# Performance work log

Measured on AMD Instinct MI355X. Metric: run time of the kernel, lower is better.

The kernel has to match this reference:

```python
import jax, jax.numpy as jnp
import numpy as np

N_SHOTS, N_SAMPLES, IMG = 10, 192, 256
M = N_SHOTS * N_SAMPLES  # 1920 k-space samples


def _radial_traj():
    # mri-nufft initialize_2D_radial: uniform spoke angles over pi,
    # radii in [-0.5, 0.5) with N_SAMPLES points per spoke.
    r = (np.arange(N_SAMPLES) - N_SAMPLES / 2) / N_SAMPLES
    ang = np.pi * np.arange(N_SHOTS) / N_SHOTS
    kx = np.cos(ang)[:, None] * r[None, :]
    ky = np.sin(ang)[:, None] * r[None, :]
    return np.stack([kx, ky], axis=-1).reshape(-1, 2).astype(np.float32)


def _phase_mats(samples):
    # Separable NDFT phase factors: exp(-2i*pi*k_x*i), exp(-2i*pi*k_y*j)
    grid = jnp.arange(IMG, dtype=jnp.float32) - IMG / 2  # centered pixel coords
    Ax = jnp.exp(-2j * jnp.pi * samples[:, 0:1] * grid[None, :]).astype(jnp.complex64)  # (M, IMG)
    Ay = jnp.exp(-2j * jnp.pi * samples[:, 1:2] * grid[None, :]).astype(jnp.complex64)  # (M, IMG)
    return Ax, Ay


def _pipe_density(samples, n_iter=10):
    # Pipe & Menon density compensation: w <- w / |F F^H w| (density=True in gpunufft).
    Ax, Ay = _phase_mats(samples)
    w = jnp.ones(M, jnp.complex64)
    for _ in range(n_iter):
        t = Ax.conj() * w[:, None]                    # (M, IMG)
        img = jnp.einsum('mi,mj->ij', t, Ay.conj())   # F^H w, (IMG, IMG)
        back = jnp.einsum('mi,ij,mj->m', Ax, img, Ay) # F F^H w, (M,)
        w = w / jnp.maximum(jnp.abs(back), 1e-12).astype(jnp.complex64)
    return jnp.abs(w).astype(jnp.float32)


def setup_inputs() -> dict:
    key = jax.random.key(0)
    k1, k2 = jax.random.split(key)
    B, C = 64, 1
    x_real = jax.random.normal(k1, (B, C, IMG, IMG), dtype=jnp.float32)
    x_imag = jax.random.normal(k2, (B, C, IMG, IMG), dtype=jnp.float32)
    samples = jnp.asarray(_radial_traj())
    density = _pipe_density(samples)
    return {"x_real": x_real, "x_imag": x_imag, "samples": samples, "density": density}


def reference(x_real, x_imag, samples, density):
    x = (x_real + 1j * x_imag).astype(jnp.complex64)  # (B, C, IMG, IMG)
    Ax, Ay = _phase_mats(samples)
    # Forward NUFFT (type-2 NDFT): kspace[b,c,m] = sum_ij Ax[m,i] Ay[m,j] x[b,c,i,j]
    t = jnp.einsum('mi,bcij->bcmj', Ax, x)            # (B, C, M, IMG)
    kspace = jnp.einsum('mj,bcmj->bcm', Ay, t)        # (B, C, M)
    # Density-compensated adjoint NUFFT (type-1 NDFT)
    kw = kspace * density.astype(jnp.complex64)
    u = jnp.einsum('mi,bcm->bcmi', Ax.conj(), kw)     # (B, C, M, IMG)
    adj = jnp.einsum('mj,bcmi->bcij', Ay.conj(), u) / (IMG * IMG)
    return jnp.stack([adj.real, adj.imag], axis=-1)   # (B, C, IMG, IMG, 2)
```

## Files before the change

kernel.cpp:

```cpp
#include <hip/hip_runtime.h>
#include <hip/hip_fp16.h>

constexpr int IMG_ = 256;
constexpr int M_   = 1920;
constexpr int B_   = 64;
constexpr int MI_  = M_ * IMG_;
constexpr int IMG2 = IMG_ * IMG_;

typedef _Float16 half8 __attribute__((ext_vector_type(8)));
typedef float floatx16 __attribute__((ext_vector_type(16)));

__device__ inline void gl_lds16(const void* g, void* l) {
  __builtin_amdgcn_global_load_lds(
      (const __attribute__((address_space(1))) unsigned int*)g,
      (__attribute__((address_space(3))) unsigned int*)l, 16, 0, 0);
}

__global__ __launch_bounds__(256) void phase1_k(
    const float* __restrict__ samples,
    _Float16* __restrict__ axh_r, _Float16* __restrict__ axh_i,
    _Float16* __restrict__ ayh_r, _Float16* __restrict__ ayh_i) {
  int idx = blockIdx.x * 256 + threadIdx.x;
  if (idx >= MI_) return;
  int m = idx >> 8;
  int i = idx & 255;
  float g  = (float)i - 128.0f;
  float kx = samples[2 * m + 0];
  float ky = samples[2 * m + 1];
  float sx, cx, sy, cy;
  sincospif(-2.0f * kx * g, &sx, &cx);
  sincospif(-2.0f * ky * g, &sy, &cy);
  axh_r[idx] = (_Float16)cx; axh_i[idx] = (_Float16)sx;
  ayh_r[idx] = (_Float16)cy; ayh_i[idx] = (_Float16)sy;
}

__global__ __launch_bounds__(256) void phase2_k(
    const float* __restrict__ samples,
    _Float16* __restrict__ axtc_r, _Float16* __restrict__ axtc_i,
    _Float16* __restrict__ aytc_r, _Float16* __restrict__ aytc_i) {
  int m = blockIdx.x * 256 + threadIdx.x;
  if (m >= M_) return;
  int i = blockIdx.y;
  float g  = (float)i - 128.0f;
  float kx = samples[2 * m + 0];
  float ky = samples[2 * m + 1];
  float sx, cx, sy, cy;
  sincospif(-2.0f * kx * g, &sx, &cx);
  sincospif(-2.0f * ky * g, &sy, &cy);
  int o = i * M_ + m;
  axtc_r[o] = (_Float16)cx; axtc_i[o] = (_Float16)(-sx);
  aytc_r[o] = (_Float16)cy; aytc_i[o] = (_Float16)(-sy);
}

__global__ __launch_bounds__(256) void xcvt_k(
    const float* __restrict__ xr, const float* __restrict__ xi,
    _Float16* __restrict__ xh_r, _Float16* __restrict__ xh_i) {
  int idx = (blockIdx.x * 256 + threadIdx.x) * 8;
  float4 a = *(const float4*)&xr[idx];
  float4 c = *(const float4*)&xr[idx + 4];
  half8 h;
  h[0] = (_Float16)a.x; h[1] = (_Float16)a.y; h[2] = (_Float16)a.z; h[3] = (_Float16)a.w;
  h[4] = (_Float16)c.x; h[5] = (_Float16)c.y; h[6] = (_Float16)c.z; h[7] = (_Float16)c.w;
  *(half8*)&xh_r[idx] = h;
  a = *(const float4*)&xi[idx];
  c = *(const float4*)&xi[idx + 4];
  h[0] = (_Float16)a.x; h[1] = (_Float16)a.y; h[2] = (_Float16)a.z; h[3] = (_Float16)a.w;
  h[4] = (_Float16)c.x; h[5] = (_Float16)c.y; h[6] = (_Float16)c.z; h[7] = (_Float16)c.w;
  *(half8*)&xh_i[idx] = h;
}

__global__ __launch_bounds__(256, 2) void fwd_k(
    const _Float16* __restrict__ axh_r, const _Float16* __restrict__ axh_i,
    const _Float16* __restrict__ ayh_r, const _Float16* __restrict__ ayh_i,
    const _Float16* __restrict__ xh_r, const _Float16* __restrict__ xh_i,
    const float* __restrict__ density,
    _Float16* __restrict__ kwh_r, _Float16* __restrict__ kwh_i) {
  __shared__ _Float16 sA[2][2 * 128 * 32];
  __shared__ _Float16 sB[2][2 * 128 * 32];
  __shared__ float kred[2][128][2];

  const int t  = threadIdx.x;
  const int w  = t >> 6, l = t & 63;
  const int lo = l & 31, hi = l >> 5;
  const int mw  = (w & 1) * 64;
  const int iwb = w >> 1;
  const int iw  = iwb * 64;
  const int m0 = blockIdx.x * 128;
  const int b  = blockIdx.y;

  ((float*)kred)[t]       = 0.f;
  ((float*)kred)[t + 256] = 0.f;

  const _Float16* __restrict__ xbr = xh_r + (size_t)b * IMG2;
  const _Float16* __restrict__ xbi = xh_i + (size_t)b * IMG2;

  const floatx16 z16 = {0.f,0.f,0.f,0.f,0.f,0.f,0.f,0.f,0.f,0.f,0.f,0.f,0.f,0.f,0.f,0.f};
  floatx16 accr[2][2], acci[2][2];

  auto stage = [&](int kt, int buf, int ic) {
    const int j0 = kt * 32;
#pragma unroll
    for (int p = 0; p < 2; ++p) {
      int s  = w * 2 + p;
      int q  = s * 64 + l;
      int r  = q >> 2;
      int cl = (q & 3) ^ (r & 3);
      int ga = (m0 + r) * IMG_ + j0 + cl * 8;
      int gb = (ic * 128 + r) * IMG_ + j0 + cl * 8;
      gl_lds16(ayh_r + ga, &sA[buf][s * 512]);
      gl_lds16(ayh_i + ga, &sA[buf][4096 + s * 512]);
      gl_lds16(xbr + gb,  &sB[buf][s * 512]);
      gl_lds16(xbi + gb,  &sB[buf][4096 + s * 512]);
    }
  };

  auto compute = [&](int buf) {
#pragma unroll
    for (int ks = 0; ks < 2; ++ks) {
      half8 ar[2], ai[2], nai[2], br[2], bi[2];
#pragma unroll
      for (int tm = 0; tm < 2; ++tm) {
        int rt  = mw + tm * 32 + lo;
        int off = rt * 32 + ((ks * 2 + hi) ^ (rt & 3)) * 8;
        ar[tm]  = *(const half8*)&sA[buf][off];
        ai[tm]  = *(const half8*)&sA[buf][4096 + off];
        nai[tm] = -ai[tm];
      }
#pragma unroll
      for (int ti = 0; ti < 2; ++ti) {
        int rt  = iw + ti * 32 + lo;
        int off = rt * 32 + ((ks * 2 + hi) ^ (rt & 3)) * 8;
        br[ti]  = *(const half8*)&sB[buf][off];
        bi[ti]  = *(const half8*)&sB[buf][4096 + off];
      }
#pragma unroll
      for (int tm = 0; tm < 2; ++tm)
#pragma unroll
        for (int ti = 0; ti < 2; ++ti) {
          accr[tm][ti] = __builtin_amdgcn_mfma_f32_32x32x16_f16(ar[tm],  br[ti], accr[tm][ti], 0, 0, 0);
          accr[tm][ti] = __builtin_amdgcn_mfma_f32_32x32x16_f16(nai[tm], bi[ti], accr[tm][ti], 0, 0, 0);
          acci[tm][ti] = __builtin_amdgcn_mfma_f32_32x32x16_f16(ar[tm],  bi[ti], acci[tm][ti], 0, 0, 0);
          acci[tm][ti] = __builtin_amdgcn_mfma_f32_32x32x16_f16(ai[tm],  br[ti], acci[tm][ti], 0, 0, 0);
        }
    }
  };

  for (int ic = 0; ic < 2; ++ic) {
#pragma unroll
    for (int tm = 0; tm < 2; ++tm)
#pragma unroll
      for (int ti = 0; ti < 2; ++ti) { accr[tm][ti] = z16; acci[tm][ti] = z16; }

    stage(0, 0, ic);
    for (int kt = 0; kt < 8; kt += 2) {
      __syncthreads();
      stage(kt + 1, 1, ic);
      compute(0);
      __syncthreads();
      if (kt + 2 < 8) stage(kt + 2, 0, ic);
      compute(1);
    }

#pragma unroll
    for (int tm = 0; tm < 2; ++tm) {
#pragma unroll
      for (int reg = 0; reg < 16; ++reg) {
        int row = (reg & 3) + 8 * (reg >> 2) + 4 * hi;
        int m = m0 + mw + tm * 32 + row;
        float wr = 0.f, wi = 0.f;
#pragma unroll
        for (int ti = 0; ti < 2; ++ti) {
          int i = ic * 128 + iw + ti * 32 + lo;
          float xr_ = (float)axh_r[m * IMG_ + i];
          float xi_ = (float)axh_i[m * IMG_ + i];
          float tr = accr[tm][ti][reg], tv = acci[tm][ti][reg];
          wr = fmaf(xr_, tr, fmaf(-xi_, tv, wr));
          wi = fmaf(xr_, tv, fmaf(xi_, tr, wi));
        }
#pragma unroll
        for (int off = 1; off < 32; off <<= 1) {
          wr += __shfl_xor(wr, off);
          wi += __shfl_xor(wi, off);
        }
        if (lo == 0) {
          int ml = mw + tm * 32 + row;
          kred[iwb][ml][0] += wr;
          kred[iwb][ml][1] += wi;
        }
      }
    }
  }

  __syncthreads();
  if (t < 128) {
    int m = m0 + t;
    float rr = kred[0][t][0] + kred[1][t][0];
    float ii = kred[0][t][1] + kred[1][t][1];
    float d  = density[m];
    kwh_r[b * M_ + m] = (_Float16)(rr * d);
    kwh_i[b * M_ + m] = (_Float16)(ii * d);
  }
}

__global__ __launch_bounds__(512, 2) void adj_k(
    const _Float16* __restrict__ axtc_r, const _Float16* __restrict__ axtc_i,
    const _Float16* __restrict__ aytc_r, const _Float16* __restrict__ aytc_i,
    const _Float16* __restrict__ kwh_r, const _Float16* __restrict__ kwh_i,
    float* __restrict__ out) {
  __shared__ _Float16 sA[2][2 * 128 * 32];
  __shared__ _Float16 sB[2][2 * 128 * 32];

  const int t  = threadIdx.x;
  const int w  = t >> 6, l = t & 63;
  const int lo = l & 31, hi = l >> 5;
  const int iw = (w & 1) * 64;
  const int jw = (w >> 1) * 32;
  const int i0 = blockIdx.x * 128;
  const int j0 = blockIdx.y * 128;
  const int b  = blockIdx.z;

  const floatx16 z16 = {0.f,0.f,0.f,0.f,0.f,0.f,0.f,0.f,0.f,0.f,0.f,0.f,0.f,0.f,0.f,0.f};
  floatx16 accr[2] = {z16, z16};
  floatx16 acci[2] = {z16, z16};

  auto stage = [&](int mt, int buf) {
    const int m0 = mt * 32;
#pragma unroll
    for (int p = 0; p < 2; ++p) {
      int s   = w * 2 + p;
      int arr = s >> 3, sl = s & 7;
      int q   = sl * 64 + l;
      int r   = q >> 2;
      int cl  = (q & 3) ^ (r & 3);
      int gb  = (j0 + r) * M_ + m0 + cl * 8;
      const _Float16* src = arr ? aytc_i : aytc_r;
      gl_lds16(src + gb, &sB[buf][arr * 4096 + sl * 512]);
    }
    {
      int q  = t;
      int r  = q >> 2;
      int cl = (q & 3) ^ (r & 3);
      int ga = (i0 + r) * M_ + m0 + cl * 8;
      half8 xr8 = *(const half8*)&axtc_r[ga];
      half8 xi8 = *(const half8*)&axtc_i[ga];
      half8 kr8 = *(const half8*)&kwh_r[b * M_ + m0 + cl * 8];
      half8 ki8 = *(const half8*)&kwh_i[b * M_ + m0 + cl * 8];
      half8 wr8 = xr8 * kr8 - xi8 * ki8;
      half8 wi8 = xr8 * ki8 + xi8 * kr8;
      *(half8*)&sA[buf][q * 8]        = wr8;
      *(half8*)&sA[buf][4096 + q * 8] = wi8;
    }
  };

  auto compute = [&](int buf) {
#pragma unroll
    for (int ks = 0; ks < 2; ++ks) {
      half8 ar[2], ai[2], nai[2], br, bi;
#pragma unroll
      for (int tm = 0; tm < 2; ++tm) {
        int rt  = iw + tm * 32 + lo;
        int off = rt * 32 + ((ks * 2 + hi) ^ (rt & 3)) * 8;
        ar[tm]  = *(const half8*)&sA[buf][off];
        ai[tm]  = *(const half8*)&sA[buf][4096 + off];
        nai[tm] = -ai[tm];
      }
      {
        int rt  = jw + lo;
        int off = rt * 32 + ((ks * 2 + hi) ^ (rt & 3)) * 8;
        br = *(const half8*)&sB[buf][off];
        bi = *(const half8*)&sB[buf][4096 + off];
      }
#pragma unroll
      for (int tm = 0; tm < 2; ++tm) {
        accr[tm] = __builtin_amdgcn_mfma_f32_32x32x16_f16(ar[tm],  br, accr[tm], 0, 0, 0);
        accr[tm] = __builtin_amdgcn_mfma_f32_32x32x16_f16(nai[tm], bi, accr[tm], 0, 0, 0);
        acci[tm] = __builtin_amdgcn_mfma_f32_32x32x16_f16(ar[tm],  bi, acci[tm], 0, 0, 0);
        acci[tm] = __builtin_amdgcn_mfma_f32_32x32x16_f16(ai[tm],  br, acci[tm], 0, 0, 0);
      }
    }
  };

  stage(0, 0);
  for (int mt = 0; mt < M_ / 32; mt += 2) {
    __syncthreads();
    stage(mt + 1, 1);
    compute(0);
    __syncthreads();
    if (mt + 2 < M_ / 32) stage(mt + 2, 0);
    compute(1);
  }

  const float s = 1.0f / (float)IMG2;
#pragma unroll
  for (int tm = 0; tm < 2; ++tm)
#pragma unroll
    for (int reg = 0; reg < 16; ++reg) {
      int row = (reg & 3) + 8 * (reg >> 2) + 4 * hi;
      int ig = i0 + iw + tm * 32 + row;
      int jg = j0 + jw + lo;
      float2 v = make_float2(accr[tm][reg] * s, acci[tm][reg] * s);
      *(float2*)&out[((size_t)(b * IMG_ + ig) * IMG_ + jg) * 2] = v;
    }
}

extern "C" void kernel_launch(void* const* d_in, const int* in_sizes, int n_in,
                              void* d_out, int out_size, void* d_ws, size_t ws_size,
                              hipStream_t stream) {
  (void)in_sizes; (void)n_in; (void)out_size; (void)ws_size;

  const float* xr      = (const float*)d_in[0];
  const float* xi      = (const float*)d_in[1];
  const float* samples = (const float*)d_in[2];
  const float* density = (const float*)d_in[3];
  float* out = (float*)d_out;

  _Float16* f = (_Float16*)d_ws;
  _Float16* axh_r  = f + 0 * MI_;
  _Float16* axh_i  = f + 1 * MI_;
  _Float16* ayh_r  = f + 2 * MI_;
  _Float16* ayh_i  = f + 3 * MI_;
  _Float16* axtc_r = f + 4 * MI_;
  _Float16* axtc_i = f + 5 * MI_;
  _Float16* aytc_r = f + 6 * MI_;
  _Float16* aytc_i = f + 7 * MI_;
  _Float16* kwh_r  = f + 8 * MI_;
  _Float16* kwh_i  = kwh_r + B_ * M_;

  _Float16* xh_r = (_Float16*)d_out;
  _Float16* xh_i = xh_r + (size_t)B_ * IMG2;

  phase1_k<<<(MI_ + 255) / 256, 256, 0, stream>>>(samples, axh_r, axh_i, ayh_r, ayh_i);
  phase2_k<<<dim3(8, IMG_), 256, 0, stream>>>(samples, axtc_r, axtc_i, aytc_r, aytc_i);
  xcvt_k<<<(B_ * IMG2) / 8 / 256, 256, 0, stream>>>(xr, xi, xh_r, xh_i);
  fwd_k<<<dim3(M_ / 128, B_), 256, 0, stream>>>(axh_r, axh_i, ayh_r, ayh_i,
                                                xh_r, xh_i, density, kwh_r, kwh_i);
  adj_k<<<dim3(2, 2, B_), 512, 0, stream>>>(axtc_r, axtc_i, aytc_r, aytc_i,
                                            kwh_r, kwh_i, out);
}
```

Baseline: 302.0 us.

## Retile adjoint kernel to 256 threads, prefetch A into registers, rotate LDS swizzle

```diff
diff --git a/kernel.cpp b/kernel.cpp
--- a/kernel.cpp
+++ b/kernel.cpp
@@ -15,6 +15,7 @@
       (const __attribute__((address_space(1))) unsigned int*)g,
       (__attribute__((address_space(3))) unsigned int*)l, 16, 0, 0);
 }
+
 
 __global__ __launch_bounds__(256) void phase1_k(
     const float* __restrict__ samples,
@@ -104,7 +105,7 @@
       int s  = w * 2 + p;
       int q  = s * 64 + l;
       int r  = q >> 2;
-      int cl = (q & 3) ^ (r & 3);
+      int cl = ((q & 3) - ((q >> 3) & 3)) & 3;
       int ga = (m0 + r) * IMG_ + j0 + cl * 8;
       int gb = (ic * 128 + r) * IMG_ + j0 + cl * 8;
       gl_lds16(ayh_r + ga, &sA[buf][s * 512]);
@@ -117,11 +118,12 @@
   auto compute = [&](int buf) {
 #pragma unroll
     for (int ks = 0; ks < 2; ++ks) {
+      const int k = ks * 2 + hi;
       half8 ar[2], ai[2], nai[2], br[2], bi[2];
 #pragma unroll
       for (int tm = 0; tm < 2; ++tm) {
         int rt  = mw + tm * 32 + lo;
-        int off = rt * 32 + ((ks * 2 + hi) ^ (rt & 3)) * 8;
+        int off = rt * 32 + ((( rt >> 1) + k) & 3) * 8;
         ar[tm]  = *(const half8*)&sA[buf][off];
         ai[tm]  = *(const half8*)&sA[buf][4096 + off];
         nai[tm] = -ai[tm];
@@ -129,7 +131,7 @@
 #pragma unroll
       for (int ti = 0; ti < 2; ++ti) {
         int rt  = iw + ti * 32 + lo;
-        int off = rt * 32 + ((ks * 2 + hi) ^ (rt & 3)) * 8;
+        int off = rt * 32 + ((( rt >> 1) + k) & 3) * 8;
         br[ti]  = *(const half8*)&sB[buf][off];
         bi[ti]  = *(const half8*)&sB[buf][4096 + off];
       }
@@ -202,13 +204,13 @@
   }
 }
 
-__global__ __launch_bounds__(512, 2) void adj_k(
+__global__ __launch_bounds__(256, 2) void adj_k(
     const _Float16* __restrict__ axtc_r, const _Float16* __restrict__ axtc_i,
     const _Float16* __restrict__ aytc_r, const _Float16* __restrict__ aytc_i,
     const _Float16* __restrict__ kwh_r, const _Float16* __restrict__ kwh_i,
     float* __restrict__ out) {
   __shared__ _Float16 sA[2][2 * 128 * 32];
-  __shared__ _Float16 sB[2][2 * 128 * 32];
+  __shared__ _Float16 sB[2][2 * 64 * 32];
 
   const int t  = threadIdx.x;
   const int w  = t >> 6, l = t & 63;
@@ -216,59 +218,72 @@
   const int iw = (w & 1) * 64;
   const int jw = (w >> 1) * 32;
   const int i0 = blockIdx.x * 128;
-  const int j0 = blockIdx.y * 128;
+  const int j0 = blockIdx.y * 64;
   const int b  = blockIdx.z;
 
   const floatx16 z16 = {0.f,0.f,0.f,0.f,0.f,0.f,0.f,0.f,0.f,0.f,0.f,0.f,0.f,0.f,0.f,0.f};
   floatx16 accr[2] = {z16, z16};
   floatx16 acci[2] = {z16, z16};
 
-  auto stage = [&](int mt, int buf) {
+  half8 pxr[2], pxi[2], pkr[2], pki[2];
+
+  auto loadA = [&](int mt) {
     const int m0 = mt * 32;
 #pragma unroll
-    for (int p = 0; p < 2; ++p) {
-      int s   = w * 2 + p;
-      int arr = s >> 3, sl = s & 7;
-      int q   = sl * 64 + l;
-      int r   = q >> 2;
-      int cl  = (q & 3) ^ (r & 3);
+    for (int s = 0; s < 2; ++s) {
+      int rs = t + s * 256;
+      int r  = rs >> 2, p = rs & 3;
+      int cl = (p - (r >> 1)) & 3;
+      int ga = (i0 + r) * M_ + m0 + cl * 8;
+      pxr[s] = *(const half8*)&axtc_r[ga];
+      pxi[s] = *(const half8*)&axtc_i[ga];
+      pkr[s] = *(const half8*)&kwh_r[b * M_ + m0 + cl * 8];
+      pki[s] = *(const half8*)&kwh_i[b * M_ + m0 + cl * 8];
+    }
+  };
+  auto writeA = [&](int buf) {
+#pragma unroll
+    for (int s = 0; s < 2; ++s) {
+      int rs = t + s * 256;
+      half8 wr8 = pxr[s] * pkr[s] - pxi[s] * pki[s];
+      half8 wi8 = pxr[s] * pki[s] + pxi[s] * pkr[s];
+      *(half8*)&sA[buf][rs * 8]        = wr8;
+      *(half8*)&sA[buf][4096 + rs * 8] = wi8;
+    }
+  };
+  auto stageB = [&](int mt, int buf) {
+    const int m0 = mt * 32;
+#pragma unroll
+    for (int p2 = 0; p2 < 2; ++p2) {
+      int sl = w * 2 + p2;
+      int q  = sl * 64 + l;
+      int arr = q >> 8;
+      int qq  = q & 255;
+      int r   = qq >> 2, p = qq & 3;
+      int cl  = (p - (r >> 1)) & 3;
       int gb  = (j0 + r) * M_ + m0 + cl * 8;
       const _Float16* src = arr ? aytc_i : aytc_r;
-      gl_lds16(src + gb, &sB[buf][arr * 4096 + sl * 512]);
-    }
-    {
-      int q  = t;
-      int r  = q >> 2;
-      int cl = (q & 3) ^ (r & 3);
-      int ga = (i0 + r) * M_ + m0 + cl * 8;
-      half8 xr8 = *(const half8*)&axtc_r[ga];
-      half8 xi8 = *(const half8*)&axtc_i[ga];
-      half8 kr8 = *(const half8*)&kwh_r[b * M_ + m0 + cl * 8];
-      half8 ki8 = *(const half8*)&kwh_i[b * M_ + m0 + cl * 8];
-      half8 wr8 = xr8 * kr8 - xi8 * ki8;
-      half8 wi8 = xr8 * ki8 + xi8 * kr8;
-      *(half8*)&sA[buf][q * 8]        = wr8;
-      *(half8*)&sA[buf][4096 + q * 8] = wi8;
-    }
-  };
-
+      gl_lds16(src + gb, &sB[buf][sl * 512]);
+    }
+  };
   auto compute = [&](int buf) {
 #pragma unroll
     for (int ks = 0; ks < 2; ++ks) {
+      const int k = ks * 2 + hi;
       half8 ar[2], ai[2], nai[2], br, bi;
 #pragma unroll
       for (int tm = 0; tm < 2; ++tm) {
         int rt  = iw + tm * 32 + lo;
-        int off = rt * 32 + ((ks * 2 + hi) ^ (rt & 3)) * 8;
+        int off = rt * 32 + (((rt >> 1) + k) & 3) * 8;
         ar[tm]  = *(const half8*)&sA[buf][off];
         ai[tm]  = *(const half8*)&sA[buf][4096 + off];
         nai[tm] = -ai[tm];
       }
       {
         int rt  = jw + lo;
-        int off = rt * 32 + ((ks * 2 + hi) ^ (rt & 3)) * 8;
+        int off = rt * 32 + (((rt >> 1) + k) & 3) * 8;
         br = *(const half8*)&sB[buf][off];
-        bi = *(const half8*)&sB[buf][4096 + off];
+        bi = *(const half8*)&sB[buf][2048 + off];
       }
 #pragma unroll
       for (int tm = 0; tm < 2; ++tm) {
@@ -280,14 +295,18 @@
     }
   };
 
-  stage(0, 0);
-  for (int mt = 0; mt < M_ / 32; mt += 2) {
+  loadA(0);
+  stageB(0, 0);
+  writeA(0);
+  for (int mt = 0; mt < M_ / 32; ++mt) {
+    const int cur = mt & 1, nxt = cur ^ 1;
     __syncthreads();
-    stage(mt + 1, 1);
-    compute(0);
-    __syncthreads();
-    if (mt + 2 < M_ / 32) stage(mt + 2, 0);
-    compute(1);
+    if (mt + 1 < M_ / 32) {
+      loadA(mt + 1);
+      stageB(mt + 1, nxt);
+    }
+    compute(cur);
+    if (mt + 1 < M_ / 32) writeA(nxt);
   }
 
   const float s = 1.0f / (float)IMG2;
@@ -334,6 +353,6 @@
   xcvt_k<<<(B_ * IMG2) / 8 / 256, 256, 0, stream>>>(xr, xi, xh_r, xh_i);
   fwd_k<<<dim3(M_ / 128, B_), 256, 0, stream>>>(axh_r, axh_i, ayh_r, ayh_i,
                                                 xh_r, xh_i, density, kwh_r, kwh_i);
-  adj_k<<<dim3(2, 2, B_), 512, 0, stream>>>(axtc_r, axtc_i, aytc_r, aytc_i,
+  adj_k<<<dim3(2, 4, B_), 256, 0, stream>>>(axtc_r, axtc_i, aytc_r, aytc_i,
                                             kwh_r, kwh_i, out);
 }
```

Result: no change. 302.9 us (+0.3%).
